# Optimization experiments

Hardware: AMD Instinct MI355X
Metric: run time of the kernel (lower is better)

Reference implementation:

```python
import jax, jax.numpy as jnp
import numpy as np

N_NODES = 50000   # number of graph nodes
N_EDGES = 800000  # avg degree 16
D_IN = 128
D_OUT = 128


def setup_inputs() -> dict:
    key = jax.random.key(0)
    k = jax.random.split(key, 5)
    seq = jax.random.normal(k[0], (N_NODES, D_IN), dtype=jnp.float32)
    # Linear weight, torch layout [out_dim, in_dim], xavier-ish scale
    W = jax.random.normal(k[1], (D_OUT, D_IN), dtype=jnp.float32) * (1.414 / np.sqrt(D_IN))
    b = jnp.zeros((D_OUT,), dtype=jnp.float32)  # bias init fill_(0.0)
    # COO sparse adjacency: out[row] += val * seq_proj[col]
    edge_row = jax.random.randint(k[2], (N_EDGES,), 0, N_NODES, dtype=jnp.int32)
    edge_col = jax.random.randint(k[3], (N_EDGES,), 0, N_NODES, dtype=jnp.int32)
    edge_val = jax.random.uniform(k[4], (N_EDGES,), dtype=jnp.float32)
    return {"seq": seq, "W": W, "b": b,
            "edge_row": edge_row, "edge_col": edge_col, "edge_val": edge_val}


def reference(seq, W, b, edge_row, edge_col, edge_val):
    # seq = self.fc(seq): [N, D_in] @ [D_in, D_out]
    h = seq @ W.T                                   # [N, D_out]
    # out = torch.spmm(adj, h): COO gather-scale-scatter
    msgs = h[edge_col] * edge_val[:, None]          # [E, D_out]
    out = jax.ops.segment_sum(msgs, edge_row, num_segments=N_NODES)  # [N, D_out]
    # bias add + relu (fused epilogue)
    return jax.nn.relu(out + b)
```

## Files before the change

kernel.cpp:

```cpp
#include <hip/hip_runtime.h>

#define NN 50000
#define NE 800000
#define DD 128

#define BK_SHIFT 8
#define NBUCK 196
#define ECAP 8192
#define CHUNK 2048
#define NCHUNK 391
#define NGB 782
#define BROWS 64
#define RCAP 2048

#define OFF_H      0
#define OFF_EBIN   3200000
#define OFF_CUR    6411264
#define WS_FULL_FLOATS 6411460

typedef short short8 __attribute__((ext_vector_type(8)));
typedef float f32x4 __attribute__((ext_vector_type(4)));

static __device__ __forceinline__ unsigned int f2bf(float x) {
    unsigned int u = __float_as_uint(x);
    return (u + 0x7fffu + ((u >> 16) & 1u)) >> 16;
}

__global__ __launch_bounds__(256) void k1_scatter_gemm(
        const float* __restrict__ seq, const float* __restrict__ W,
        unsigned short* __restrict__ h,
        const int* __restrict__ erow, const int* __restrict__ ecol,
        const float* __restrict__ eval,
        int* __restrict__ gcur, uint2* __restrict__ ebin) {
    __shared__ uint4 lds4[3072];
    char* lds = (char*)lds4;
    const int t = threadIdx.x;

    if (blockIdx.x < NCHUNK) {
        int* lh = (int*)lds4;
        for (int i = t; i < NBUCK; i += 256) lh[i] = 0;
        __syncthreads();
        const int e0 = blockIdx.x * CHUNK;
        for (int i = t; i < CHUNK; i += 256) {
            int e = e0 + i;
            if (e < NE) atomicAdd(&lh[erow[e] >> BK_SHIFT], 1);
        }
        __syncthreads();
        for (int i = t; i < NBUCK; i += 256) {
            int c = lh[i];
            lh[i] = c ? atomicAdd(&gcur[i], c) : 0;
        }
        __syncthreads();
        for (int i = t; i < CHUNK; i += 256) {
            int e = e0 + i;
            if (e < NE) {
                int r = erow[e], c = ecol[e];
                unsigned int vb = __float_as_uint(eval[e]);
                int k = r >> BK_SHIFT;
                int pos = atomicAdd(&lh[k], 1);
                if (pos < ECAP)
                    ebin[(size_t)k * ECAP + pos] =
                        make_uint2(((unsigned)r << 16) | (unsigned)c, vb);
            }
        }
        return;
    }

    const int base = (blockIdx.x - NCHUNK) * 64;
#define BS_OFF 16384

    {
        const int o = t >> 1, ksb = (t & 1) * 64;
        const float4* Wr = (const float4*)(W + o * 128 + ksb);
#pragma unroll
        for (int i = 0; i < 16; i += 2) {
            float4 x = Wr[i], y = Wr[i + 1];
            uint4 p;
            p.x = f2bf(x.x) | (f2bf(x.y) << 16);
            p.y = f2bf(x.z) | (f2bf(x.w) << 16);
            p.z = f2bf(y.x) | (f2bf(y.y) << 16);
            p.w = f2bf(y.z) | (f2bf(y.w) << 16);
            int byte = o * 256 + (ksb + i * 4) * 2;
            *(uint4*)(lds + BS_OFF + (byte ^ ((o & 7) << 4))) = p;
        }
    }
    {
        const int row = t >> 2, n = base + row;
        const int c0 = (t & 3) * 4;
        const float4* Sr = (const float4*)(seq + (size_t)n * 128);
        const bool ok = (n < NN);
#pragma unroll
        for (int i = 0; i < 4; ++i) {
            int cc = c0 + i;
            float4 x = ok ? Sr[cc * 2]     : make_float4(0.f, 0.f, 0.f, 0.f);
            float4 y = ok ? Sr[cc * 2 + 1] : make_float4(0.f, 0.f, 0.f, 0.f);
            uint4 p;
            p.x = f2bf(x.x) | (f2bf(x.y) << 16);
            p.y = f2bf(x.z) | (f2bf(x.w) << 16);
            p.z = f2bf(y.x) | (f2bf(y.y) << 16);
            p.w = f2bf(y.z) | (f2bf(y.w) << 16);
            int byte = row * 256 + cc * 16;
            *(uint4*)(lds + (byte ^ ((row & 7) << 4))) = p;
        }
    }
    __syncthreads();

    const int l = t & 63, wv = t >> 6;
    const int lr = l & 15, kg = l >> 4;
    const int arow = wv * 16 + lr;
    f32x4 acc[8] = {};

#pragma unroll
    for (int ks = 0; ks < 4; ++ks) {
        const int kbyte = ks * 64 + kg * 16;
        short8 av = *(short8*)(lds + ((arow * 256 + kbyte) ^ ((arow & 7) << 4)));
#pragma unroll
        for (int c = 0; c < 8; ++c) {
            const int o = c * 16 + lr;
            short8 bv = *(short8*)(lds + BS_OFF +
                                   ((o * 256 + kbyte) ^ ((o & 7) << 4)));
            acc[c] = __builtin_amdgcn_mfma_f32_16x16x32_bf16(av, bv, acc[c], 0, 0, 0);
        }
    }

#pragma unroll
    for (int c = 0; c < 8; ++c) {
#pragma unroll
        for (int r = 0; r < 4; ++r) {
            int n = base + wv * 16 + kg * 4 + r;
            if (n < NN)
                h[(size_t)n * DD + c * 16 + lr] = (unsigned short)f2bf(acc[c][r]);
        }
    }
}

__global__ __launch_bounds__(512) void k2_fill_gather(
        const unsigned short* __restrict__ h,
        const uint2* __restrict__ ebin,
        const int* __restrict__ gcur,
        const float* __restrict__ bias,
        float* __restrict__ out) {
    __shared__ unsigned int recs[RCAP];
    __shared__ int lh[BROWS];
    __shared__ int rend[BROWS];
    __shared__ int rcur[BROWS];
    const int t = threadIdx.x;
    const int kc = blockIdx.x >> 2;
    const int s  = blockIdx.x & 3;
    const int wid = t >> 6, lane = t & 63;

    int cnt = gcur[kc];
    if (cnt > ECAP) cnt = ECAP;
    const uint2* eb = ebin + (size_t)kc * ECAP;

    if (t < BROWS) lh[t] = 0;
    __syncthreads();
    for (int e = t; e < cnt; e += 512) {
        int row = (int)(eb[e].x >> 16);
        if (((row >> 6) & 3) == s) atomicAdd(&lh[row & (BROWS - 1)], 1);
    }
    __syncthreads();
    if (t < BROWS) {
        int x = lh[t];
#pragma unroll
        for (int off = 1; off < 64; off <<= 1) {
            int y = __shfl_up(x, off);
            if (lane >= off) x += y;
        }
        if (x > RCAP) x = RCAP;
        rend[t] = x;
        rcur[t] = x - lh[t];
    }
    __syncthreads();
    for (int e = t; e < cnt; e += 512) {
        uint2 ed = eb[e];
        int row = (int)(ed.x >> 16);
        if (((row >> 6) & 3) == s) {
            int pos = atomicAdd(&rcur[row & (BROWS - 1)], 1);
            if (pos < RCAP)
                recs[pos] = (ed.x & 0xffffu) | (f2bf(__uint_as_float(ed.y)) << 16);
        }
    }
    __syncthreads();

    const int slot = lane >> 4;
    const int sub  = lane & 15;
    const unsigned short* hp = h + sub * 8;
    const float4* b4 = (const float4*)(bias + sub * 8);
    const float4 b0 = b4[0], b1 = b4[1];

#define BODY(EE) do {                                                          \
        unsigned int cv = recs[EE];                                            \
        float v = __uint_as_float(cv & 0xffff0000u);                           \
        uint4 hv = *(const uint4*)(hp + (size_t)(cv & 0xffffu) * DD);          \
        unsigned int uu;                                                       \
        uu = hv.x;                                                             \
        acc[0] = fmaf(v, __uint_as_float(uu << 16),          acc[0]);          \
        acc[1] = fmaf(v, __uint_as_float(uu & 0xffff0000u),  acc[1]);          \
        uu = hv.y;                                                             \
        acc[2] = fmaf(v, __uint_as_float(uu << 16),          acc[2]);          \
        acc[3] = fmaf(v, __uint_as_float(uu & 0xffff0000u),  acc[3]);          \
        uu = hv.z;                                                             \
        acc[4] = fmaf(v, __uint_as_float(uu << 16),          acc[4]);          \
        acc[5] = fmaf(v, __uint_as_float(uu & 0xffff0000u),  acc[5]);          \
        uu = hv.w;                                                             \
        acc[6] = fmaf(v, __uint_as_float(uu << 16),          acc[6]);          \
        acc[7] = fmaf(v, __uint_as_float(uu & 0xffff0000u),  acc[7]);          \
    } while (0)

#pragma unroll 1
    for (int ri = 0; ri < 8; ++ri) {
        const int row = wid * 8 + ri;
        const int begin = row ? rend[row - 1] : 0;
        const int e1 = rend[row];
        float acc[8] = {0.f, 0.f, 0.f, 0.f, 0.f, 0.f, 0.f, 0.f};

        int e = begin + slot;
        for (; e + 12 < e1; e += 16) { BODY(e); BODY(e + 4); BODY(e + 8); BODY(e + 12); }
        for (; e < e1; e += 4) BODY(e);

#pragma unroll
        for (int i = 0; i < 8; ++i) {
            acc[i] += __shfl_xor(acc[i], 16);
            acc[i] += __shfl_xor(acc[i], 32);
        }

        if (slot == 0) {
            const int n = blockIdx.x * BROWS + row;
            if (n < NN) {
                f32x4 o0, o1;
                o0.x = fmaxf(acc[0] + b0.x, 0.f);
                o0.y = fmaxf(acc[1] + b0.y, 0.f);
                o0.z = fmaxf(acc[2] + b0.z, 0.f);
                o0.w = fmaxf(acc[3] + b0.w, 0.f);
                o1.x = fmaxf(acc[4] + b1.x, 0.f);
                o1.y = fmaxf(acc[5] + b1.y, 0.f);
                o1.z = fmaxf(acc[6] + b1.z, 0.f);
                o1.w = fmaxf(acc[7] + b1.w, 0.f);
                f32x4* op = (f32x4*)(out + (size_t)n * DD + sub * 8);
                __builtin_nontemporal_store(o0, op);
                __builtin_nontemporal_store(o1, op + 1);
            }
        }
    }
#undef BODY
}

extern "C" void kernel_launch(void* const* d_in, const int* in_sizes, int n_in,
                              void* d_out, int out_size, void* d_ws, size_t ws_size,
                              hipStream_t stream) {
    const float* seq  = (const float*)d_in[0];
    const float* W    = (const float*)d_in[1];
    const float* b    = (const float*)d_in[2];
    const int*   erow = (const int*)d_in[3];
    const int*   ecol = (const int*)d_in[4];
    const float* eval = (const float*)d_in[5];
    float* out = (float*)d_out;

    float* wsf = (float*)d_ws;
    unsigned short* h = (unsigned short*)(wsf + OFF_H);
    uint2* ebin = (uint2*)(wsf + OFF_EBIN);
    int*   gcur = (int*)(wsf + OFF_CUR);

    hipMemsetAsync(gcur, 0, NBUCK * sizeof(int), stream);
    k1_scatter_gemm<<<NCHUNK + NGB, 256, 0, stream>>>(seq, W, h, erow, ecol,
                                                      eval, gcur, ebin);
    k2_fill_gather<<<NBUCK * 4, 512, 0, stream>>>(h, ebin, gcur, b, out);
}
```

Measured before the change: 71.85 us.

## Cache edge rows in registers and compact bucket edges into LDS in one pass

In the scatter phase, each block now handles twice as many edges (16 per thread) and keeps the row indices in registers, so erow is read once instead of twice. In the gather kernel, the two global passes over each bucket's edge list become one: a ballot-based wave compaction writes the matching records and their row ids into LDS staging buffers, and a second pass scatters them into row order from LDS. The aim is to halve global reads of the edge bins and erow. The cost is more LDS per block and more registers, and the scatter phase now runs with half as many blocks.

```diff
diff --git a/kernel.cpp b/kernel.cpp
--- a/kernel.cpp
+++ b/kernel.cpp
@@ -7,8 +7,9 @@
 #define BK_SHIFT 8
 #define NBUCK 196
 #define ECAP 8192
-#define CHUNK 2048
-#define NCHUNK 391
+#define CHUNK 4096
+#define NCHUNK 196
+#define EPT 16
 #define NGB 782
 #define BROWS 64
 #define RCAP 2048
@@ -38,12 +39,15 @@
 
     if (blockIdx.x < NCHUNK) {
         int* lh = (int*)lds4;
+        int rbuf[EPT];
         for (int i = t; i < NBUCK; i += 256) lh[i] = 0;
         __syncthreads();
         const int e0 = blockIdx.x * CHUNK;
-        for (int i = t; i < CHUNK; i += 256) {
-            int e = e0 + i;
-            if (e < NE) atomicAdd(&lh[erow[e] >> BK_SHIFT], 1);
+#pragma unroll
+        for (int j = 0; j < EPT; ++j) {
+            int e = e0 + j * 256 + t;
+            rbuf[j] = (e < NE) ? erow[e] : -1;
+            if (rbuf[j] >= 0) atomicAdd(&lh[rbuf[j] >> BK_SHIFT], 1);
         }
         __syncthreads();
         for (int i = t; i < NBUCK; i += 256) {
@@ -51,11 +55,13 @@
             lh[i] = c ? atomicAdd(&gcur[i], c) : 0;
         }
         __syncthreads();
-        for (int i = t; i < CHUNK; i += 256) {
-            int e = e0 + i;
-            if (e < NE) {
-                int r = erow[e], c = ecol[e];
+#pragma unroll
+        for (int j = 0; j < EPT; ++j) {
+            int r = rbuf[j];
+            if (r >= 0) {
+                int e = e0 + j * 256 + t;
                 unsigned int vb = __float_as_uint(eval[e]);
+                int c = ecol[e];
                 int k = r >> BK_SHIFT;
                 int pos = atomicAdd(&lh[k], 1);
                 if (pos < ECAP)
@@ -141,9 +147,12 @@
         const float* __restrict__ bias,
         float* __restrict__ out) {
     __shared__ unsigned int recs[RCAP];
+    __shared__ unsigned int rtmp[RCAP];
+    __shared__ unsigned char rowb[RCAP];
     __shared__ int lh[BROWS];
     __shared__ int rend[BROWS];
     __shared__ int rcur[BROWS];
+    __shared__ int tot;
     const int t = threadIdx.x;
     const int kc = blockIdx.x >> 2;
     const int s  = blockIdx.x & 3;
@@ -153,13 +162,32 @@
     if (cnt > ECAP) cnt = ECAP;
     const uint2* eb = ebin + (size_t)kc * ECAP;
 
+    if (t == 0) tot = 0;
     if (t < BROWS) lh[t] = 0;
     __syncthreads();
-    for (int e = t; e < cnt; e += 512) {
-        int row = (int)(eb[e].x >> 16);
-        if (((row >> 6) & 3) == s) atomicAdd(&lh[row & (BROWS - 1)], 1);
-    }
-    __syncthreads();
+
+    for (int e0 = 0; e0 < cnt; e0 += 512) {
+        int e = e0 + t;
+        uint2 ed = (e < cnt) ? eb[e] : make_uint2(0u, 0u);
+        int row = (int)(ed.x >> 16);
+        bool ok = (e < cnt) && (((row >> 6) & 3) == s);
+        unsigned long long m = __ballot(ok);
+        int wcnt = __popcll(m);
+        int b0 = 0;
+        if (lane == 0 && wcnt) b0 = atomicAdd(&tot, wcnt);
+        b0 = __shfl(b0, 0);
+        if (ok) {
+            int pos = b0 + __popcll(m & ((1ull << lane) - 1ull));
+            int r6 = row & (BROWS - 1);
+            if (pos < RCAP) {
+                rtmp[pos] = (ed.x & 0xffffu) | (f2bf(__uint_as_float(ed.y)) << 16);
+                rowb[pos] = (unsigned char)r6;
+            }
+            atomicAdd(&lh[r6], 1);
+        }
+    }
+    __syncthreads();
+
     if (t < BROWS) {
         int x = lh[t];
 #pragma unroll
@@ -172,14 +200,12 @@
         rcur[t] = x - lh[t];
     }
     __syncthreads();
-    for (int e = t; e < cnt; e += 512) {
-        uint2 ed = eb[e];
-        int row = (int)(ed.x >> 16);
-        if (((row >> 6) & 3) == s) {
-            int pos = atomicAdd(&rcur[row & (BROWS - 1)], 1);
-            if (pos < RCAP)
-                recs[pos] = (ed.x & 0xffffu) | (f2bf(__uint_as_float(ed.y)) << 16);
-        }
+
+    int nt = tot < RCAP ? tot : RCAP;
+    for (int i = t; i < nt; i += 512) {
+        int r6 = rowb[i];
+        int pos = atomicAdd(&rcur[r6], 1);
+        if (pos < RCAP) recs[pos] = rtmp[i];
     }
     __syncthreads();
 
@@ -187,7 +213,7 @@
     const int sub  = lane & 15;
     const unsigned short* hp = h + sub * 8;
     const float4* b4 = (const float4*)(bias + sub * 8);
-    const float4 b0 = b4[0], b1 = b4[1];
+    const float4 b0v = b4[0], b1v = b4[1];
 
 #define BODY(EE) do {                                                          \
         unsigned int cv = recs[EE];                                            \
@@ -229,14 +255,14 @@
             const int n = blockIdx.x * BROWS + row;
             if (n < NN) {
                 f32x4 o0, o1;
-                o0.x = fmaxf(acc[0] + b0.x, 0.f);
-                o0.y = fmaxf(acc[1] + b0.y, 0.f);
-                o0.z = fmaxf(acc[2] + b0.z, 0.f);
-                o0.w = fmaxf(acc[3] + b0.w, 0.f);
-                o1.x = fmaxf(acc[4] + b1.x, 0.f);
-                o1.y = fmaxf(acc[5] + b1.y, 0.f);
-                o1.z = fmaxf(acc[6] + b1.z, 0.f);
-                o1.w = fmaxf(acc[7] + b1.w, 0.f);
+                o0.x = fmaxf(acc[0] + b0v.x, 0.f);
+                o0.y = fmaxf(acc[1] + b0v.y, 0.f);
+                o0.z = fmaxf(acc[2] + b0v.z, 0.f);
+                o0.w = fmaxf(acc[3] + b0v.w, 0.f);
+                o1.x = fmaxf(acc[4] + b1v.x, 0.f);
+                o1.y = fmaxf(acc[5] + b1v.y, 0.f);
+                o1.z = fmaxf(acc[6] + b1v.z, 0.f);
+                o1.w = fmaxf(acc[7] + b1v.w, 0.f);
                 f32x4* op = (f32x4*)(out + (size_t)n * DD + sub * 8);
                 __builtin_nontemporal_store(o0, op);
                 __builtin_nontemporal_store(o1, op + 1);
```

Result: faster. 69.74 us, median of 2 (-2.9%).
